# Performance work log

Measured on AMD Instinct MI355X. Metric: run time of the kernel, lower is better.

Reference implementation:

```python
import jax, jax.numpy as jnp
import numpy as np

WIN = 7                      # window_size[0] == window_size[1]
N_TOK = WIN * WIN            # 49 tokens per window
PRETRAIN = 12                # pretrain_window_size
LOG8 = float(np.log(8.0))


def _relative_position_index():
    # tf.meshgrid default 'xy' indexing == np.meshgrid default
    gh, gw = np.meshgrid(np.arange(WIN), np.arange(WIN))
    coords = np.stack([gh, gw], 0).reshape(2, -1)            # [2, N]
    rel = coords[:, :, None] - coords[:, None, :]            # [2, N, N]
    rel = rel.transpose(1, 2, 0)                             # [N, N, 2]
    ry = (rel[..., 0] + WIN - 1) * (2 * WIN - 1)
    rx = rel[..., 1] + WIN - 1
    return jnp.asarray((ry + rx).reshape(-1), dtype=jnp.int32)   # [N*N]


def _relative_coords_table():
    ch = np.arange(-(WIN - 1), WIN, dtype=np.float32)
    gh, gw = np.meshgrid(ch, ch)                             # 'xy' indexing
    t = np.stack([gh, gw], axis=-1)[None]                    # [1, 2W-1, 2W-1, 2]
    t = t / (PRETRAIN - 1)                                   # first divide
    t = t * (8.0 / (PRETRAIN - 1))                           # scale (as in source)
    t = np.sign(t) * np.log1p(np.abs(t)) / LOG8
    return jnp.asarray(t, dtype=jnp.float32)


REL_IDX = _relative_position_index()
COORDS_TABLE = _relative_coords_table()


def _l2_normalize(t, eps=1e-12):
    return t * jax.lax.rsqrt(jnp.maximum(jnp.sum(t * t, axis=-1, keepdims=True), eps))


def setup_inputs() -> dict:
    key = jax.random.key(0)
    ks = jax.random.split(key, 12)
    Bw, N, C, H, RPE_H = 2048, N_TOK, 512, 16, 512
    s = 0.02
    return {
        "x": jax.random.normal(ks[0], (Bw, N, C), jnp.float32),
        "mask": jax.random.normal(ks[1], (64, N, N), jnp.float32),
        "qkv_w": jax.random.normal(ks[2], (C, 3 * C), jnp.float32) * s,
        "q_bias": jnp.zeros((C,), jnp.float32),
        "v_bias": jnp.zeros((C,), jnp.float32),
        "logit_scale": jnp.full((H, 1, 1), np.log(10.0), jnp.float32),
        "rpe_w1": jax.random.normal(ks[3], (2, RPE_H), jnp.float32) * s,
        "rpe_b1": jnp.zeros((RPE_H,), jnp.float32),
        "rpe_w2": jax.random.normal(ks[4], (RPE_H, H), jnp.float32) * s,
        "proj_w": jax.random.normal(ks[5], (C, C), jnp.float32) * s,
        "proj_b": jnp.zeros((C,), jnp.float32),
    }


def reference(x, mask, qkv_w, q_bias, v_bias, logit_scale,
              rpe_w1, rpe_b1, rpe_w2, proj_w, proj_b):
    Bw, N, C = x.shape
    H = logit_scale.shape[0]
    hd = C // H

    qkv_bias = jnp.concatenate([q_bias, jnp.zeros_like(v_bias), v_bias])
    qkv = x @ qkv_w + qkv_bias                          # [Bw, N, 3C]
    qkv = qkv.reshape(Bw, N, 3, H, hd).transpose(2, 0, 3, 1, 4)
    q, k, v = qkv[0], qkv[1], qkv[2]                    # [Bw, H, N, hd]

    scale = jnp.exp(jnp.minimum(logit_scale, jnp.log(1.0 / 0.01)))  # [H,1,1]
    q = _l2_normalize(q)
    k = _l2_normalize(k)
    attn = jnp.einsum('bhnd,bhmd->bhnm', q, k) * scale  # [Bw, H, N, N]

    # RPE MLP on the (2W-1)^2 coords table, then gather per token pair
    h1 = jax.nn.relu(COORDS_TABLE @ rpe_w1 + rpe_b1)
    bias_table = (h1 @ rpe_w2).reshape(-1, H)           # [(2W-1)^2, H]
    pb = bias_table[REL_IDX].reshape(N, N, H).transpose(2, 0, 1)  # [H, N, N]
    attn = attn + 16.0 * jax.nn.sigmoid(pb)[None]

    nW = mask.shape[0]
    attn = attn.reshape(Bw // nW, nW, H, N, N) + mask[None, :, None]
    attn = attn.reshape(Bw, H, N, N)

    attn = jax.nn.softmax(attn, axis=-1)
    out = jnp.einsum('bhnm,bhmd->bnhd', attn, v).reshape(Bw, N, C)
    return out @ proj_w + proj_b
```

## Files before the change

kernel.cpp:

```cpp
#include <hip/hip_runtime.h>
#include <cstdint>

#define NTOK 49
#define CDIM 512
#define BW 2048
#define MROWS (BW * NTOK)
#define QKVN 1536

typedef __attribute__((ext_vector_type(4))) float f32x4;
typedef __attribute__((ext_vector_type(8))) short s16x8;
typedef __attribute__((ext_vector_type(2))) unsigned int u32x2;

__device__ __forceinline__ uint16_t f2b(float f) {
  uint32_t u = __float_as_uint(f);
  u += 0x7fffu + ((u >> 16) & 1u);
  return (uint16_t)(u >> 16);
}
__device__ __forceinline__ float b2f(uint16_t h) {
  return __uint_as_float(((uint32_t)h) << 16);
}

#define GLOAD_LDS16(gp, lp)                                                    \
  __builtin_amdgcn_global_load_lds(                                            \
      (__attribute__((address_space(1))) void*)(gp),                           \
      (__attribute__((address_space(3))) void*)(lp), 16, 0, 0)

__global__ __launch_bounds__(256) void cvt_x_kernel(const float* __restrict__ x,
                                                    uint16_t* __restrict__ xb) {
  long i = ((long)blockIdx.x * 256 + threadIdx.x) * 4;
  f32x4 v = *(const f32x4*)(x + i);
  uint64_t p = (uint64_t)f2b(v[0]) | ((uint64_t)f2b(v[1]) << 16) |
               ((uint64_t)f2b(v[2]) << 32) | ((uint64_t)f2b(v[3]) << 48);
  *(uint64_t*)(xb + i) = p;
}

__global__ __launch_bounds__(256) void prep_weights(
    const float* __restrict__ qkv_w, const float* __restrict__ proj_w,
    const float* __restrict__ q_bias, const float* __restrict__ v_bias,
    uint16_t* __restrict__ qkv_wT, uint16_t* __restrict__ proj_wT,
    float* __restrict__ qkv_bias) {
  int i = blockIdx.x * 256 + threadIdx.x;
  if (i < QKVN * CDIM) {
    int nn = i / CDIM, kk = i % CDIM;
    qkv_wT[i] = f2b(qkv_w[(long)kk * QKVN + nn]);
  }
  if (i < CDIM * CDIM) {
    int nn = i / CDIM, kk = i % CDIM;
    proj_wT[i] = f2b(proj_w[(long)kk * CDIM + nn]);
  }
  if (i < QKVN) {
    float bv = (i < 512) ? q_bias[i] : (i < 1024 ? 0.f : v_bias[i - 1024]);
    qkv_bias[i] = bv;
  }
}

__global__ __launch_bounds__(256) void rpe_table(const float* __restrict__ w1,
                                                 const float* __restrict__ b1,
                                                 const float* __restrict__ w2,
                                                 float* __restrict__ bias16) {
  int i = blockIdx.x * 256 + threadIdx.x;
  if (i >= 169 * 16) return;
  int f = i >> 4, h = i & 15;
  float d0 = (float)((f % 13) - 6);
  float d1 = (float)((f / 13) - 6);
  const float inv_log8 = 0.4808983469629878f;
  float v0 = (d0 / 11.0f) * (8.0f / 11.0f);
  float v1 = (d1 / 11.0f) * (8.0f / 11.0f);
  float f0 = copysignf(log1pf(fabsf(v0)) * inv_log8, v0);
  if (v0 == 0.f) f0 = 0.f;
  float f1 = copysignf(log1pf(fabsf(v1)) * inv_log8, v1);
  if (v1 == 0.f) f1 = 0.f;
  float acc = 0.f;
  for (int k = 0; k < 512; ++k) {
    float h1 = fmaxf(f0 * w1[k] + f1 * w1[512 + k] + b1[k], 0.f);
    acc += h1 * w2[k * 16 + h];
  }
  bias16[i] = 16.f / (1.f + expf(-acc));
}

__global__ __launch_bounds__(256) void build_tiles(
    const float* __restrict__ mask, const float* __restrict__ bias16,
    float* __restrict__ mask_t, float* __restrict__ bias_t) {
  int bid = blockIdx.x;
  int l = threadIdx.x >> 2, j = threadIdx.x & 3;
  int gg = l >> 4, cc = l & 15;
  if (bid < 1024) {
    int w = bid >> 4, tile = bid & 15;
    int mt = tile >> 2, nt = tile & 3;
    int q = nt * 16 + cc, k = mt * 16 + gg * 4 + j;
    float v;
    if (k >= 49) v = -1e30f;
    else if (q >= 49) v = 0.f;
    else v = mask[(long)w * 2401 + q * 49 + k];
    mask_t[(long)bid * 256 + threadIdx.x] = v;
  } else {
    int idx = bid - 1024;
    int h = idx >> 4, tile = idx & 15;
    int mt = tile >> 2, nt = tile & 3;
    int q = nt * 16 + cc, k = mt * 16 + gg * 4 + j;
    float v = 0.f;
    if (q < 49 && k < 49) {
      int ridx = (q % 7 - k % 7 + 6) * 13 + (q / 7 - k / 7 + 6);
      v = bias16[ridx * 16 + h];
    }
    bias_t[(long)idx * 256 + threadIdx.x] = v;
  }
}


#define STAGE_A(tile, half, buf)                                               \
  {                                                                            \
    const uint16_t* s_ = srcA + (half) * (128L * 512) + (long)(tile) * 64;     \
    uint16_t* d_ = &lds[(buf) * 32768 + (half) * 8192 + tid * 8];              \
    GLOAD_LDS16(s_, d_);                                                       \
    GLOAD_LDS16(s_ + 64 * 512, d_ + 4096);                                     \
  }

#define STAGE_B(tile, half, buf)                                               \
  {                                                                            \
    const uint16_t* s_ = srcB + (half) * (128L * 512) + (long)(tile) * 64;     \
    uint16_t* d_ = &lds[(buf) * 32768 + 16384 + (half) * 8192 + tid * 8];      \
    GLOAD_LDS16(s_, d_);                                                       \
    GLOAD_LDS16(s_ + 64 * 512, d_ + 4096);                                     \
  }

#define VM4 asm volatile("s_waitcnt vmcnt(4)" ::: "memory");
#define VM0 asm volatile("s_waitcnt vmcnt(0)" ::: "memory");

#define PHASE(buf, q, STAGES, TAIL)                                            \
  {                                                                            \
    s16x8 a00 = *(const s16x8*)&lds[(buf)*32768 + arow + (2*(q))*1024 + ax0];  \
    s16x8 a01 = *(const s16x8*)&lds[(buf)*32768 + arow + (2*(q))*1024 + ax1];  \
    s16x8 a10 = *(const s16x8*)&lds[(buf)*32768 + arow + (2*(q)+1)*1024 + ax0];\
    s16x8 a11 = *(const s16x8*)&lds[(buf)*32768 + arow + (2*(q)+1)*1024 + ax1];\
    if ((q) == 0) {                                                            \
      _Pragma("unroll")                                                        \
      for (int nf = 0; nf < 4; ++nf) {                                         \
        bfr0[nf] = *(const s16x8*)&lds[(buf)*32768 + brow_ + nf*1024 + ax0];   \
        bfr1[nf] = *(const s16x8*)&lds[(buf)*32768 + brow_ + nf*1024 + ax1];   \
      }                                                                        \
    }                                                                          \
    STAGES                                                                     \
    __builtin_amdgcn_s_barrier();                                              \
    asm volatile("s_waitcnt lgkmcnt(0)" ::: "memory");                         \
    __builtin_amdgcn_sched_barrier(0);                                         \
    __builtin_amdgcn_s_setprio(1);                                             \
    _Pragma("unroll")                                                          \
    for (int nf = 0; nf < 4; ++nf) {                                           \
      acc[2*(q)][nf] = __builtin_amdgcn_mfma_f32_16x16x32_bf16(                \
          a00, bfr0[nf], acc[2*(q)][nf], 0, 0, 0);                             \
      acc[2*(q)][nf] = __builtin_amdgcn_mfma_f32_16x16x32_bf16(                \
          a01, bfr1[nf], acc[2*(q)][nf], 0, 0, 0);                             \
      acc[2*(q)+1][nf] = __builtin_amdgcn_mfma_f32_16x16x32_bf16(              \
          a10, bfr0[nf], acc[2*(q)+1][nf], 0, 0, 0);                           \
      acc[2*(q)+1][nf] = __builtin_amdgcn_mfma_f32_16x16x32_bf16(              \
          a11, bfr1[nf], acc[2*(q)+1][nf], 0, 0, 0);                           \
    }                                                                          \
    __builtin_amdgcn_s_setprio(0);                                             \
    TAIL                                                                       \
    __builtin_amdgcn_s_barrier();                                              \
  }

template <int EPI>
__global__ __launch_bounds__(512, 2) void gemm8p(const uint16_t* __restrict__ A,
                                                 const uint16_t* __restrict__ BT,
                                                 const float* __restrict__ bias,
                                                 void* __restrict__ Cout,
                                                 int N, int ntn) {
  __shared__ uint16_t lds[2 * 32768];
  const int tid = threadIdx.x;
  const int wave = tid >> 6, lane = tid & 63;
  const int wm = wave >> 2, wn = wave & 3;
  const int c = lane & 15, g = lane >> 4;

  const int bid = blockIdx.x;
  const int nwg = gridDim.x;
  const int wg = (bid & 7) * (nwg >> 3) + (bid >> 3);
  const int mt = wg / ntn, nt = wg % ntn;
  const long brow = (long)mt * 256;
  const int bcol = nt * 256;

  const int lr0 = tid >> 3;
  const int chunk = tid & 7;
  const int scol = (chunk ^ (lr0 & 7)) * 8;
  const uint16_t* srcA = A + (brow + lr0) * 512 + scol;
  const uint16_t* srcB = BT + ((long)bcol + lr0) * 512 + scol;

  const int arow = wm * 8192 + c * 64;
  const int brow_ = 16384 + (wn >> 1) * 8192 + ((wn & 1) * 64 + c) * 64;
  const int ax0 = (g * 8) ^ ((c & 7) * 8);
  const int ax1 = (32 + g * 8) ^ ((c & 7) * 8);

  f32x4 acc[8][4];
#pragma unroll
  for (int i = 0; i < 8; ++i)
#pragma unroll
    for (int j = 0; j < 4; ++j) acc[i][j] = f32x4{0.f, 0.f, 0.f, 0.f};
  s16x8 bfr0[4], bfr1[4];

  STAGE_A(0, 0, 0); STAGE_A(0, 1, 0);
  STAGE_B(0, 0, 0); STAGE_B(0, 1, 0);
  STAGE_B(1, 0, 1); STAGE_B(1, 1, 1);
  asm volatile("s_waitcnt vmcnt(4)" ::: "memory");
  __builtin_amdgcn_s_barrier();

  for (int i = 0; i < 3; ++i) {
    const int t0 = 2 * i;
    PHASE(0, 0, STAGE_A(t0 + 1, 0, 1), )
    PHASE(0, 1, STAGE_A(t0 + 1, 1, 1), )
    PHASE(0, 2, STAGE_B(t0 + 2, 0, 0), )
    PHASE(0, 3, STAGE_B(t0 + 2, 1, 0), VM4)
    PHASE(1, 0, STAGE_A(t0 + 2, 0, 0), )
    PHASE(1, 1, STAGE_A(t0 + 2, 1, 0), )
    PHASE(1, 2, STAGE_B(t0 + 3, 0, 1), )
    PHASE(1, 3, STAGE_B(t0 + 3, 1, 1), VM4)
  }
  PHASE(0, 0, STAGE_A(7, 0, 1), )
  PHASE(0, 1, STAGE_A(7, 1, 1), )
  PHASE(0, 2, , )
  PHASE(0, 3, , VM0)
  PHASE(1, 0, , )
  PHASE(1, 1, , )
  PHASE(1, 2, , )
  PHASE(1, 3, , )

#pragma unroll
  for (int mf = 0; mf < 8; ++mf) {
#pragma unroll
    for (int nf = 0; nf < 4; ++nf) {
      const int col = bcol + wn * 64 + nf * 16 + c;
      const float bv = bias[col];
#pragma unroll
      for (int r = 0; r < 4; ++r) {
        const long grow = brow + wm * 128 + mf * 16 + g * 4 + r;
        const float v = acc[mf][nf][r] + bv;
        if (EPI == 0)
          ((uint16_t*)Cout)[grow * N + col] = f2b(v);
        else
          ((float*)Cout)[grow * N + col] = v;
      }
    }
  }
}

__global__ __launch_bounds__(256) void attn_mfma(
    const uint16_t* __restrict__ qkv,
    const float* __restrict__ logit_scale,
    const float* __restrict__ bias_t,
    const float* __restrict__ mask_t,
    uint16_t* __restrict__ outb) {
  __shared__ uint16_t Vs[4][2048];
  __shared__ uint16_t P[4][64 * 72];
  const int tid = threadIdx.x;
  const int wave = tid >> 6, lane = tid & 63;
  const int g = lane >> 4, c = lane & 15;
  const int b = blockIdx.x >> 2;
  const int h = ((blockIdx.x & 3) << 2) | wave;
  const long rbase = (long)b * 49;

  uint16_t* vdst = Vs[wave];
#pragma unroll
  for (int i = 0; i < 4; ++i) {
    int chunk = i * 64 + lane;
    int row = chunk >> 2, part = chunk & 3;
    if (row > 48) { row = 0; part = 0; }
    GLOAD_LDS16(qkv + (rbase + row) * QKVN + 1024 + h * 32 + part * 8,
                vdst + i * 512 + lane * 8);
  }

  const long qoff = rbase * QKVN + h * 32;
  s16x8 kf[4], qf[4];
#pragma unroll
  for (int t = 0; t < 4; ++t) {
    int row = t * 16 + c;
    s16x8 kv = {}, qv = {};
    if (row < 49) {
      qv = *(const s16x8*)(qkv + qoff + (long)row * QKVN + g * 8);
      kv = *(const s16x8*)(qkv + qoff + (long)row * QKVN + 512 + g * 8);
    }
    float kfv[8], qfv[8];
    float kss = 0.f, qss = 0.f;
#pragma unroll
    for (int m = 0; m < 8; ++m) {
      kfv[m] = b2f((uint16_t)kv[m]); kss += kfv[m] * kfv[m];
      qfv[m] = b2f((uint16_t)qv[m]); qss += qfv[m] * qfv[m];
    }
    kss += __shfl_xor(kss, 16); kss += __shfl_xor(kss, 32);
    qss += __shfl_xor(qss, 16); qss += __shfl_xor(qss, 32);
    float kr = rsqrtf(fmaxf(kss, 1e-12f));
    float qr = rsqrtf(fmaxf(qss, 1e-12f));
#pragma unroll
    for (int m = 0; m < 8; ++m) {
      kv[m] = (short)f2b(kfv[m] * kr);
      qv[m] = (short)f2b(qfv[m] * qr);
    }
    kf[t] = kv; qf[t] = qv;
  }

  f32x4 s[4][4];
#pragma unroll
  for (int mt = 0; mt < 4; ++mt)
#pragma unroll
    for (int nt = 0; nt < 4; ++nt)
      s[mt][nt] = __builtin_amdgcn_mfma_f32_16x16x32_bf16(
          kf[mt], qf[nt], f32x4{0.f, 0.f, 0.f, 0.f}, 0, 0, 0);

  const float scale = __expf(fminf(logit_scale[h], 4.6051702f));
  const float* bt = bias_t + (long)h * 4096;
  const float* mk = mask_t + (long)(b & 63) * 4096;
#pragma unroll
  for (int mt = 0; mt < 4; ++mt)
#pragma unroll
    for (int nt = 0; nt < 4; ++nt) {
      int tile = mt * 4 + nt;
      f32x4 eb = *(const f32x4*)(bt + tile * 256 + lane * 4);
      f32x4 em = *(const f32x4*)(mk + tile * 256 + lane * 4);
#pragma unroll
      for (int j = 0; j < 4; ++j)
        s[mt][nt][j] = s[mt][nt][j] * scale + eb[j] + em[j];
    }

#pragma unroll
  for (int nt = 0; nt < 4; ++nt) {
    float mx = -3.0e38f;
#pragma unroll
    for (int mt = 0; mt < 4; ++mt)
#pragma unroll
      for (int j = 0; j < 4; ++j) mx = fmaxf(mx, s[mt][nt][j]);
    mx = fmaxf(mx, __shfl_xor(mx, 16));
    mx = fmaxf(mx, __shfl_xor(mx, 32));
    float sum = 0.f;
#pragma unroll
    for (int mt = 0; mt < 4; ++mt)
#pragma unroll
      for (int j = 0; j < 4; ++j) {
        float e = __expf(s[mt][nt][j] - mx);
        s[mt][nt][j] = e; sum += e;
      }
    sum += __shfl_xor(sum, 16);
    sum += __shfl_xor(sum, 32);
    float inv = 1.0f / sum;
#pragma unroll
    for (int mt = 0; mt < 4; ++mt)
#pragma unroll
      for (int j = 0; j < 4; ++j) s[mt][nt][j] *= inv;
  }

  uint16_t* pw = P[wave];
#pragma unroll
  for (int mt = 0; mt < 4; ++mt)
#pragma unroll
    for (int nt = 0; nt < 4; ++nt) {
      unsigned lo = (unsigned)f2b(s[mt][nt][0]) | ((unsigned)f2b(s[mt][nt][1]) << 16);
      unsigned hi = (unsigned)f2b(s[mt][nt][2]) | ((unsigned)f2b(s[mt][nt][3]) << 16);
      int q = nt * 16 + c;
      int kb = (mt * 16 + g * 4) * 2;
      int addr = q * 144 + (kb ^ ((q & 7) << 4));
      *(u32x2*)((char*)pw + addr) = u32x2{lo, hi};
    }
  __syncthreads();

  f32x4 o[4][2];
#pragma unroll
  for (int qt = 0; qt < 4; ++qt)
#pragma unroll
    for (int dt = 0; dt < 2; ++dt) o[qt][dt] = f32x4{0.f, 0.f, 0.f, 0.f};

#pragma unroll
  for (int ks = 0; ks < 2; ++ks) {
    s16x8 vf[2];
#pragma unroll
    for (int dt = 0; dt < 2; ++dt) {
      int d = dt * 16 + c;
      s16x8 vv;
#pragma unroll
      for (int jj = 0; jj < 8; ++jj) {
        int k = ks * 32 + g * 8 + jj;
        vv[jj] = (short)vdst[k * 32 + d];
      }
      vf[dt] = vv;
    }
#pragma unroll
    for (int qt = 0; qt < 4; ++qt) {
      int q = qt * 16 + c;
      int kbyte = (ks * 64 + g * 16) ^ ((q & 7) << 4);
      s16x8 pf = *(const s16x8*)((const char*)pw + q * 144 + kbyte);
#pragma unroll
      for (int dt = 0; dt < 2; ++dt)
        o[qt][dt] = __builtin_amdgcn_mfma_f32_16x16x32_bf16(pf, vf[dt],
                                                            o[qt][dt], 0, 0, 0);
    }
  }

#pragma unroll
  for (int qt = 0; qt < 4; ++qt) {
    int q0 = qt * 16 + g * 4;
#pragma unroll
    for (int dt = 0; dt < 2; ++dt) {
      int d = dt * 16 + c;
#pragma unroll
      for (int j = 0; j < 4; ++j) {
        int q = q0 + j;
        if (q < 49)
          outb[(rbase + q) * 512 + h * 32 + d] = f2b(o[qt][dt][j]);
      }
    }
  }
}

extern "C" void kernel_launch(void* const* d_in, const int* in_sizes, int n_in,
                              void* d_out, int out_size, void* d_ws,
                              size_t ws_size, hipStream_t stream) {
  const float* x = (const float*)d_in[0];
  const float* mask = (const float*)d_in[1];
  const float* qkv_w = (const float*)d_in[2];
  const float* q_bias = (const float*)d_in[3];
  const float* v_bias = (const float*)d_in[4];
  const float* logit_scale = (const float*)d_in[5];
  const float* rpe_w1 = (const float*)d_in[6];
  const float* rpe_b1 = (const float*)d_in[7];
  const float* rpe_w2 = (const float*)d_in[8];
  const float* proj_w = (const float*)d_in[9];
  const float* proj_b = (const float*)d_in[10];

  char* ws = (char*)d_ws;
  uint16_t* xb       = (uint16_t*)ws;
  uint16_t* qkvbuf   = (uint16_t*)(ws + 102760448L);
  uint16_t* qkv_wT   = (uint16_t*)(ws + 411041792L);
  uint16_t* proj_wT  = (uint16_t*)(ws + 412614656L);
  float*    qkv_bias = (float*)(ws + 413138944L);
  float*    bias16   = (float*)(ws + 413145088L);
  float*    bias_t   = (float*)(ws + 413155904L);
  float*    mask_t   = (float*)(ws + 413418048L);

  cvt_x_kernel<<<50176, 256, 0, stream>>>(x, xb);
  prep_weights<<<3072, 256, 0, stream>>>(qkv_w, proj_w, q_bias, v_bias, qkv_wT,
                                         proj_wT, qkv_bias);
  rpe_table<<<11, 256, 0, stream>>>(rpe_w1, rpe_b1, rpe_w2, bias16);
  build_tiles<<<1280, 256, 0, stream>>>(mask, bias16, mask_t, bias_t);

  gemm8p<0><<<2352, 512, 0, stream>>>(xb, qkv_wT, qkv_bias, qkvbuf, QKVN, 6);
  attn_mfma<<<8192, 256, 0, stream>>>(qkvbuf, logit_scale, bias_t, mask_t, xb);
  gemm8p<1><<<784, 512, 0, stream>>>(xb, proj_wT, proj_b, d_out, CDIM, 2);
}
```

Baseline: 547.2 us.

## Stage bf16 GEMM epilogue through LDS, drop sched_barrier, add MFMA priority hints

Result: slower. 612.1 us (+11.9%).

```diff
diff --git a/kernel.cpp b/kernel.cpp
--- a/kernel.cpp
+++ b/kernel.cpp
@@ -143,7 +143,6 @@
     STAGES                                                                     \
     __builtin_amdgcn_s_barrier();                                              \
     asm volatile("s_waitcnt lgkmcnt(0)" ::: "memory");                         \
-    __builtin_amdgcn_sched_barrier(0);                                         \
     __builtin_amdgcn_s_setprio(1);                                             \
     _Pragma("unroll")                                                          \
     for (int nf = 0; nf < 4; ++nf) {                                           \
@@ -178,7 +177,7 @@
   const int wg = (bid & 7) * (nwg >> 3) + (bid >> 3);
   const int mt = wg / ntn, nt = wg % ntn;
   const long brow = (long)mt * 256;
-  const int bcol = nt * 256;
+  const int bcol = nt * 128 * 2;
 
   const int lr0 = tid >> 3;
   const int chunk = tid & 7;
@@ -224,20 +223,44 @@
   PHASE(1, 2, , )
   PHASE(1, 3, , )
 
-#pragma unroll
-  for (int mf = 0; mf < 8; ++mf) {
-#pragma unroll
-    for (int nf = 0; nf < 4; ++nf) {
-      const int col = bcol + wn * 64 + nf * 16 + c;
-      const float bv = bias[col];
-#pragma unroll
-      for (int r = 0; r < 4; ++r) {
-        const long grow = brow + wm * 128 + mf * 16 + g * 4 + r;
-        const float v = acc[mf][nf][r] + bv;
-        if (EPI == 0)
-          ((uint16_t*)Cout)[grow * N + col] = f2b(v);
-        else
-          ((float*)Cout)[grow * N + col] = v;
+  if (EPI == 0) {
+    uint16_t* cbuf = lds;
+    for (int p = 0; p < 2; ++p) {
+      __syncthreads();
+#pragma unroll
+      for (int mq = 0; mq < 4; ++mq) {
+        const int mf = p * 4 + mq;
+        const int lrb = wm * 64 + mq * 16 + g * 4;
+#pragma unroll
+        for (int nf = 0; nf < 4; ++nf) {
+          const int col = wn * 64 + nf * 16 + c;
+          const float bv = bias[bcol + col];
+#pragma unroll
+          for (int r = 0; r < 4; ++r)
+            cbuf[(lrb + r) * 264 + col] = f2b(acc[mf][nf][r] + bv);
+        }
+      }
+      __syncthreads();
+      const int lr2 = tid >> 2, quarter = tid & 3;
+      const long grow = brow + (lr2 >> 6) * 128 + p * 64 + (lr2 & 63);
+      uint16_t* gdst = (uint16_t*)Cout + grow * N + bcol + quarter * 64;
+      const uint16_t* lsrc = cbuf + lr2 * 264 + quarter * 64;
+#pragma unroll
+      for (int k = 0; k < 8; ++k)
+        *(f32x4*)(gdst + k * 8) = *(const f32x4*)(lsrc + k * 8);
+    }
+  } else {
+#pragma unroll
+    for (int mf = 0; mf < 8; ++mf) {
+#pragma unroll
+      for (int nf = 0; nf < 4; ++nf) {
+        const int col = bcol + wn * 64 + nf * 16 + c;
+        const float bv = bias[col];
+#pragma unroll
+        for (int r = 0; r < 4; ++r) {
+          const long grow = brow + wm * 128 + mf * 16 + g * 4 + r;
+          ((float*)Cout)[grow * N + col] = acc[mf][nf][r] + bv;
+        }
       }
     }
   }
@@ -298,12 +321,14 @@
   }
 
   f32x4 s[4][4];
+  __builtin_amdgcn_s_setprio(1);
 #pragma unroll
   for (int mt = 0; mt < 4; ++mt)
 #pragma unroll
     for (int nt = 0; nt < 4; ++nt)
       s[mt][nt] = __builtin_amdgcn_mfma_f32_16x16x32_bf16(
           kf[mt], qf[nt], f32x4{0.f, 0.f, 0.f, 0.f}, 0, 0, 0);
+  __builtin_amdgcn_s_setprio(0);
 
   const float scale = __expf(fminf(logit_scale[h], 4.6051702f));
   const float* bt = bias_t + (long)h * 4096;
@@ -380,6 +405,7 @@
       }
       vf[dt] = vv;
     }
+    __builtin_amdgcn_s_setprio(1);
 #pragma unroll
     for (int qt = 0; qt < 4; ++qt) {
       int q = qt * 16 + c;
@@ -390,6 +416,7 @@
         o[qt][dt] = __builtin_amdgcn_mfma_f32_16x16x32_bf16(pf, vf[dt],
                                                             o[qt][dt], 0, 0, 0);
     }
+    __builtin_amdgcn_s_setprio(0);
   }
 
 #pragma unroll
```
